# Performance work log

Hardware: AMD Instinct MI355X
Metric: run time of the kernel (lower is better)

Reference implementation:

```python
import jax, jax.numpy as jnp
import numpy as np

B, S, DIM, H = 2, 2048, 1024, 16
HD = DIM // H  # head dim = 64


def setup_inputs() -> dict:
    key = jax.random.key(0)
    ks = jax.random.split(key, 10)
    scale = 1.0 / np.sqrt(DIM)
    x = jax.random.normal(ks[0], (B, S, DIM), dtype=jnp.float32)
    # per-head projection weights stacked over heads: [H, DIM, HD]
    Wq = jax.random.normal(ks[1], (H, DIM, HD), dtype=jnp.float32) * scale
    bq = jax.random.normal(ks[2], (H, HD), dtype=jnp.float32) * 0.01
    Wk = jax.random.normal(ks[3], (H, DIM, HD), dtype=jnp.float32) * scale
    bk = jax.random.normal(ks[4], (H, HD), dtype=jnp.float32) * 0.01
    Wv = jax.random.normal(ks[5], (H, DIM, HD), dtype=jnp.float32) * scale
    bv = jax.random.normal(ks[6], (H, HD), dtype=jnp.float32) * 0.01
    # output linear: [DIM, DIM]
    Wo = jax.random.normal(ks[7], (DIM, DIM), dtype=jnp.float32) * scale
    bo = jax.random.normal(ks[8], (DIM,), dtype=jnp.float32) * 0.01
    return {"x": x, "Wq": Wq, "bq": bq, "Wk": Wk, "bk": bk,
            "Wv": Wv, "bv": bv, "Wo": Wo, "bo": bo}


def reference(x, Wq, bq, Wk, bk, Wv, bv, Wo, bo):
    # per-head projections: [B, H, S, HD]
    q = jnp.einsum('bsd,hde->bhse', x, Wq) + bq[None, :, None, :]
    k = jnp.einsum('bsd,hde->bhse', x, Wk) + bk[None, :, None, :]
    v = jnp.einsum('bsd,hde->bhse', x, Wv) + bv[None, :, None, :]
    # causal attention scores: [B, H, S, S], scaled by sqrt(head_dim)
    scores = jnp.einsum('bhse,bhte->bhst', q, k) / jnp.sqrt(jnp.float32(HD))
    causal = jnp.tril(jnp.ones((S, S), dtype=bool))
    scores = jnp.where(causal[None, None], scores, -jnp.inf)
    attn = jax.nn.softmax(scores, axis=-1)
    out = jnp.einsum('bhst,bhte->bhse', attn, v)  # [B, H, S, HD]
    # concat heads in order -> [B, S, DIM]
    out = out.transpose(0, 2, 1, 3).reshape(B, S, DIM)
    return out @ Wo + bo
```

## Files before the change

### kernel.cpp

```cpp
#include <hip/hip_runtime.h>

typedef _Float16 half8 __attribute__((ext_vector_type(8)));
typedef _Float16 half4 __attribute__((ext_vector_type(4)));
typedef float f32x4 __attribute__((ext_vector_type(4)));

#define MFMA32(a, b, c) __builtin_amdgcn_mfma_f32_16x16x32_f16((a), (b), (c), 0, 0, 0)
#define MFMA16(a, b, c) __builtin_amdgcn_mfma_f32_16x16x16f16((a), (b), (c), 0, 0, 0)

static constexpr int Bc = 2, Sc = 2048, DIMc = 1024, Hc = 16, HDc = 64;
static constexpr int Mc = Bc * Sc;
static constexpr int NQKV = 3 * DIMc;

__device__ __forceinline__ void gl_lds16(const _Float16* g, _Float16* l) {
  __builtin_amdgcn_global_load_lds(
      (const __attribute__((address_space(1))) void*)g,
      (__attribute__((address_space(3))) void*)l, 16, 0, 0);
}


__global__ __launch_bounds__(256) void k_prep_all(
    const float* __restrict__ x, const float* __restrict__ Wq,
    const float* __restrict__ Wk, const float* __restrict__ Wv,
    const float* __restrict__ Wo, _Float16* __restrict__ xh,
    _Float16* __restrict__ WallT, _Float16* __restrict__ WoT) {
  __shared__ float Ls[64 * 65];
  const int bx = blockIdx.x, tid = threadIdx.x;
  if (bx < 16384) {
    int i = bx * 256 + tid;
    xh[i] = (_Float16)x[i];
    return;
  }
  int b2 = bx - 16384;
  if (b2 < 768) {
    const int dt = b2 & 15, ph = b2 >> 4;
    const int p = ph >> 4, h = ph & 15;
    const float* W = (p == 0) ? Wq : (p == 1) ? Wk : Wv;
    for (int c = tid; c < 4096; c += 256) {
      int dr = c >> 6, e = c & 63;
      Ls[e * 65 + dr] = W[h * 65536 + (dt * 64 + dr) * 64 + e];
    }
    __syncthreads();
    for (int c = tid; c < 4096; c += 256) {
      int e = c >> 6, dr = c & 63;
      WallT[(size_t)(p * 1024 + h * 64 + e) * 1024 + dt * 64 + dr] = (_Float16)Ls[e * 65 + dr];
    }
  } else {
    int b3 = b2 - 768;
    const int dt = b3 & 15, nt = b3 >> 4;
    for (int c = tid; c < 4096; c += 256) {
      int dr = c >> 6, nl = c & 63;
      Ls[nl * 65 + dr] = Wo[(dt * 64 + dr) * 1024 + nt * 64 + nl];
    }
    __syncthreads();
    for (int c = tid; c < 4096; c += 256) {
      int nl = c >> 6, dr = c & 63;
      WoT[(size_t)(nt * 64 + nl) * 1024 + dt * 64 + dr] = (_Float16)Ls[nl * 65 + dr];
    }
  }
}


#define GEMM_CORE()                                                            \
  __shared__ _Float16 As[128 * 64];                                            \
  __shared__ _Float16 Bs[128 * 64];                                            \
  const int tid = threadIdx.x;                                                 \
  const int lane = tid & 63, wave = tid >> 6;                                  \
  const int quad = lane >> 4, mr = lane & 15, m7 = mr & 7;                     \
  const int wm = wave >> 1, wn = wave & 1;                                     \
  f32x4 acc[4][4];                                                             \
  for (int i = 0; i < 4; i++)                                                  \
    for (int j = 0; j < 4; j++) acc[i][j] = f32x4{0.f, 0.f, 0.f, 0.f};         \
  for (int k0 = 0; k0 < DIMc; k0 += 64) {                                      \
    __syncthreads();                                                           \
    for (int it = 0; it < 4; ++it) {                                           \
      int idx = it * 256 + tid;                                                \
      int row = idx >> 3, scb = (idx & 7) ^ (row & 7);                         \
      gl_lds16(&A[(size_t)(m0 + row) * DIMc + k0 + scb * 8],                   \
               &As[(it * 256 + wave * 64) * 8]);                               \
    }                                                                          \
    for (int it = 0; it < 4; ++it) {                                           \
      int idx = it * 256 + tid;                                                \
      int row = idx >> 3, scb = (idx & 7) ^ (row & 7);                         \
      gl_lds16(&Bt[(size_t)(n0 + row) * DIMc + k0 + scb * 8],                  \
               &Bs[(it * 256 + wave * 64) * 8]);                               \
    }                                                                          \
    __syncthreads();                                                           \
    for (int kk = 0; kk < 2; ++kk) {                                           \
      half8 af[4], bf[4];                                                      \
      for (int i = 0; i < 4; i++)                                              \
        af[i] = *(const half8*)&As[(wm * 64 + i * 16 + mr) * 64 +              \
                                   (((kk * 4 + quad) ^ m7) * 8)];              \
      for (int i = 0; i < 4; i++)                                              \
        bf[i] = *(const half8*)&Bs[(wn * 64 + i * 16 + mr) * 64 +              \
                                   (((kk * 4 + quad) ^ m7) * 8)];              \
      for (int i = 0; i < 4; i++)                                              \
        for (int j = 0; j < 4; j++) acc[i][j] = MFMA32(af[i], bf[j], acc[i][j]); \
    }                                                                          \
  }

__global__ __launch_bounds__(256) void k_gemm_qkv(
    const _Float16* __restrict__ xh, const _Float16* __restrict__ WallT,
    const float* __restrict__ bq, const float* __restrict__ bk,
    const float* __restrict__ bv, _Float16* __restrict__ qh,
    _Float16* __restrict__ kh, _Float16* __restrict__ vT) {
  const int id = blockIdx.x;
  const bool qkrole = id < 512;
  const _Float16* A;
  const _Float16* Bt;
  int m0, n0;
  if (qkrole) {
    A = xh; Bt = WallT;
    n0 = (id & 15) * 128; m0 = (id >> 4) * 128;
  } else {
    int j = id - 512;
    A = WallT + (size_t)2048 * DIMc; Bt = xh;
    n0 = (j & 31) * 128; m0 = (j >> 5) * 128;
  }
  GEMM_CORE()
  if (qkrole) {
    for (int i = 0; i < 4; i++) {
      for (int j = 0; j < 4; j++) {
        int col = n0 + wn * 64 + j * 16 + mr;
        int p = col >> 10, rem = col & 1023;
        const float* bias = p ? bk : bq;
        _Float16* dst = p ? kh : qh;
        float bb = bias[rem];
        int h = rem >> 6, e = rem & 63;
        for (int r = 0; r < 4; r++) {
          int row = m0 + wm * 64 + i * 16 + quad * 4 + r;
          int b = row >> 11, s = row & 2047;
          dst[(((size_t)(b * Hc + h)) * Sc + s) * HDc + e] = (_Float16)(acc[i][j][r] + bb);
        }
      }
    }
  } else {
    for (int i = 0; i < 4; i++) {
      int rowb = m0 + wm * 64 + i * 16 + quad * 4;
      for (int j = 0; j < 4; j++) {
        int col = n0 + wn * 64 + j * 16 + mr;
        int b = col >> 11, s = col & 2047;
        for (int r = 0; r < 4; r++) {
          int row = rowb + r;
          vT[(size_t)(b * 1024 + row) * Sc + s] = (_Float16)(acc[i][j][r] + bv[row]);
        }
      }
    }
  }
}

__global__ __launch_bounds__(256) void k_gemm_out(
    const _Float16* __restrict__ A, const _Float16* __restrict__ Bt,
    const float* __restrict__ bo, float* __restrict__ out) {
  const int m0 = blockIdx.y * 128, n0 = blockIdx.x * 128;
  GEMM_CORE()
  for (int i = 0; i < 4; i++) {
    for (int j = 0; j < 4; j++) {
      int col = n0 + wn * 64 + j * 16 + mr;
      float bb = bo[col];
      for (int r = 0; r < 4; r++) {
        int row = m0 + wm * 64 + i * 16 + quad * 4 + r;
        out[(size_t)row * DIMc + col] = acc[i][j][r] + bb;
      }
    }
  }
}


__global__ __launch_bounds__(256, 1) void k_attn(
    const _Float16* __restrict__ qg, const _Float16* __restrict__ kg,
    const _Float16* __restrict__ vTg, _Float16* __restrict__ att) {
  const int bid = blockIdx.x;
  const int qt = 31 - (bid >> 5);
  const int bh = bid & 31;
  const int b = bh >> 4, h = bh & 15;
  const int tid = threadIdx.x, w = tid >> 6, lane = tid & 63;
  const int quad = lane >> 4, mr = lane & 15, m7 = mr & 7;
  const size_t base = (size_t)bh * (Sc * HDc);
  const size_t vbase = ((size_t)b * 1024 + h * 64) * Sc;

  __shared__ _Float16 KV[4][2][2][64 * 64];
  __shared__ float Lsh[4][64];

  const int q0 = qt * 64;
  const int myn = (qt >= w) ? ((qt - w) >> 2) + 1 : 0;

  const _Float16 qsc = (_Float16)(0.125f * 1.44269504f);
  half8 aq[4][2];
  for (int qf = 0; qf < 4; ++qf)
    for (int c = 0; c < 2; ++c) {
      half8 v = *(const half8*)&qg[base + (size_t)(q0 + qf * 16 + mr) * 64 + c * 32 + quad * 8];
      for (int j = 0; j < 8; ++j) v[j] = v[j] * qsc;
      aq[qf][c] = v;
    }

  f32x4 o[4][4];
  f32x4 ol[4];
  for (int nf = 0; nf < 4; ++nf)
    for (int qf = 0; qf < 4; ++qf) o[nf][qf] = f32x4{0.f, 0.f, 0.f, 0.f};
  for (int qf = 0; qf < 4; ++qf) ol[qf] = f32x4{0.f, 0.f, 0.f, 0.f};
  const half4 ones = {(_Float16)1.f, (_Float16)1.f, (_Float16)1.f, (_Float16)1.f};

  if (myn > 0) {
    const _Float16* ks = kg + base + (size_t)w * 4096;
    const _Float16* vs = vTg + vbase + w * 64;
    for (int it = 0; it < 8; ++it) {
      int idx = it * 64 + lane;
      int row = idx >> 3, scb = (idx & 7) ^ (row & 7);
      gl_lds16(ks + (size_t)row * 64 + scb * 8, &KV[w][0][0][it * 512]);
    }
    for (int it = 0; it < 8; ++it) {
      int idx = it * 64 + lane;
      int row = idx >> 3, scb = (idx & 7) ^ (row & 7);
      gl_lds16(vs + (size_t)row * Sc + scb * 8, &KV[w][0][1][it * 512]);
    }
  }
  asm volatile("s_waitcnt vmcnt(0)" ::: "memory");

  for (int i = 0; i < myn; ++i) {
    const int t = w + (i << 2);
    const _Float16* Kc = &KV[w][i & 1][0][0];
    const _Float16* Vc = &KV[w][i & 1][1][0];

    if (i + 1 < myn) {
      const _Float16* ks = kg + base + (size_t)(t + 4) * 4096;
      const _Float16* vs = vTg + vbase + (t + 4) * 64;
      _Float16* Kn = &KV[w][(i + 1) & 1][0][0];
      _Float16* Vn = &KV[w][(i + 1) & 1][1][0];
      for (int it = 0; it < 8; ++it) {
        int idx = it * 64 + lane;
        int row = idx >> 3, scb = (idx & 7) ^ (row & 7);
        gl_lds16(ks + (size_t)row * 64 + scb * 8, Kn + it * 512);
      }
      for (int it = 0; it < 8; ++it) {
        int idx = it * 64 + lane;
        int row = idx >> 3, scb = (idx & 7) ^ (row & 7);
        gl_lds16(vs + (size_t)row * Sc + scb * 8, Vn + it * 512);
      }
    }

    const bool diag = (t == qt);
    half4 pf[4][4];
    for (int kf = 0; kf < 4; ++kf) {
      const int r0 = (kf * 16 + mr) * 64;
      half8 k0 = *(const half8*)&Kc[r0 + ((quad ^ m7) * 8)];
      half8 k1 = *(const half8*)&Kc[r0 + (((quad ^ 4) ^ m7) * 8)];
      for (int qf = 0; qf < 4; ++qf) {
        f32x4 z = {0.f, 0.f, 0.f, 0.f};
        z = MFMA32(k0, aq[qf][0], z);
        z = MFMA32(k1, aq[qf][1], z);
        half4 pp;
        const int kvb = kf * 16 + quad * 4;
        for (int r = 0; r < 4; ++r) {
          float p = __builtin_amdgcn_exp2f(z[r]);
          if (diag && (kvb + r > qf * 16 + mr)) p = 0.f;
          pp[r] = (_Float16)p;
        }
        pf[qf][kf] = pp;
      }
    }

    for (int nf = 0; nf < 4; ++nf) {
      const int er = (nf * 16 + mr) * 64;
      for (int kc = 0; kc < 4; ++kc) {
        int kb = kc * 2 + (quad >> 1);
        half4 vv = *(const half4*)&Vc[er + ((kb ^ m7) * 8) + (quad & 1) * 4];
        for (int qf = 0; qf < 4; ++qf) o[nf][qf] = MFMA16(vv, pf[qf][kc], o[nf][qf]);
      }
    }
    for (int kc = 0; kc < 4; ++kc)
      for (int qf = 0; qf < 4; ++qf) ol[qf] = MFMA16(ones, pf[qf][kc], ol[qf]);

    asm volatile("s_waitcnt vmcnt(0)" ::: "memory");
  }

  __syncthreads();
  float* Osh = (float*)&KV[0][0][0][0];
  for (int nf = 0; nf < 4; ++nf)
    for (int qf = 0; qf < 4; ++qf)
      for (int r = 0; r < 4; ++r)
        Osh[w * 4096 + (nf * 16 + quad * 4 + r) * 64 + qf * 16 + mr] = o[nf][qf][r];
  if (quad == 0)
    for (int qf = 0; qf < 4; ++qf) Lsh[w][qf * 16 + mr] = ol[qf][0];
  __syncthreads();

  const int q = tid & 63, e0 = (tid >> 6) * 16;
  const float linv = 1.0f / (Lsh[0][q] + Lsh[1][q] + Lsh[2][q] + Lsh[3][q]);
  half8 o0, o1;
  for (int e = 0; e < 8; ++e) {
    float s = Osh[(e0 + e) * 64 + q] + Osh[4096 + (e0 + e) * 64 + q] +
              Osh[8192 + (e0 + e) * 64 + q] + Osh[12288 + (e0 + e) * 64 + q];
    o0[e] = (_Float16)(s * linv);
  }
  for (int e = 8; e < 16; ++e) {
    float s = Osh[(e0 + e) * 64 + q] + Osh[4096 + (e0 + e) * 64 + q] +
              Osh[8192 + (e0 + e) * 64 + q] + Osh[12288 + (e0 + e) * 64 + q];
    o1[e - 8] = (_Float16)(s * linv);
  }
  const size_t orow = ((size_t)(b * Sc + q0 + q)) * DIMc + h * 64 + e0;
  *(half8*)&att[orow] = o0;
  *(half8*)&att[orow + 8] = o1;
}


extern "C" void kernel_launch(void* const* d_in, const int* in_sizes, int n_in,
                              void* d_out, int out_size, void* d_ws, size_t ws_size,
                              hipStream_t stream) {
  const float* x  = (const float*)d_in[0];
  const float* Wq = (const float*)d_in[1];
  const float* bq = (const float*)d_in[2];
  const float* Wk = (const float*)d_in[3];
  const float* bk = (const float*)d_in[4];
  const float* Wv = (const float*)d_in[5];
  const float* bv = (const float*)d_in[6];
  const float* Wo = (const float*)d_in[7];
  const float* bo = (const float*)d_in[8];
  float* out = (float*)d_out;

  _Float16* p = (_Float16*)d_ws;
  _Float16* xh    = p; p += (size_t)Mc * DIMc;
  _Float16* WallT = p; p += (size_t)NQKV * DIMc;
  _Float16* WoT   = p; p += (size_t)DIMc * DIMc;
  _Float16* qh    = p; p += (size_t)Bc * Hc * Sc * HDc;
  _Float16* kh    = p; p += (size_t)Bc * Hc * Sc * HDc;
  _Float16* vT    = p; p += (size_t)Bc * Hc * Sc * HDc;
  _Float16* atth  = p;

  k_prep_all<<<16384 + 768 + 256, 256, 0, stream>>>(x, Wq, Wk, Wv, Wo, xh, WallT, WoT);
  k_gemm_qkv<<<768, 256, 0, stream>>>(xh, WallT, bq, bk, bv, qh, kh, vT);
  k_attn<<<1024, 256, 0, stream>>>(qh, kh, vT, atth);
  k_gemm_out<<<dim3(DIMc / 128, Mc / 128), 256, 0, stream>>>(atth, WoT, bo, out);
}
```

Measured before the change: 212.3 us.

## Load K/V fragments directly into registers instead of staging through LDS

Attention now reads K and V fragments straight from global memory into registers, with K double-buffered in registers across ping-pong unrolled tiles, instead of async-copying swizzled tiles into LDS. The score/exp and PV MFMAs are interleaved per 16-key chunk, which shrinks the live probability array. LDS use drops to the final reduction buffer and launch bounds allow two blocks per CU, aiming to cut LDS traffic and raise occupancy. In exchange, V loads become strided half4 global reads, and register pressure under the tighter launch bound may cause spills.

```diff
diff --git a/kernel.cpp b/kernel.cpp
--- a/kernel.cpp
+++ b/kernel.cpp
@@ -166,7 +166,44 @@
 }
 
 
-__global__ __launch_bounds__(256, 1) void k_attn(
+#define ATT_TILE(KC, KN, tt)                                                   \
+  {                                                                            \
+    const int t_ = (tt);                                                       \
+    if (t_ + 4 <= qt) {                                                        \
+      for (int kf = 0; kf < 4; ++kf) {                                         \
+        const size_t r_ = (size_t)((t_ + 4) * 64 + kf * 16 + mr) * 64;         \
+        KN[kf][0] = *(const half8*)&Kg[r_ + quad * 8];                         \
+        KN[kf][1] = *(const half8*)&Kg[r_ + 32 + quad * 8];                    \
+      }                                                                        \
+    }                                                                          \
+    half4 vv[4][4];                                                            \
+    for (int nf = 0; nf < 4; ++nf)                                             \
+      for (int kc = 0; kc < 4; ++kc)                                           \
+        vv[nf][kc] = *(const half4*)&Vg[(size_t)(nf * 16 + mr) * Sc +          \
+                                        t_ * 64 + kc * 16 + quad * 4];         \
+    const bool diag = (t_ == qt);                                              \
+    for (int kc = 0; kc < 4; ++kc) {                                           \
+      half4 pf4[4];                                                            \
+      for (int qf = 0; qf < 4; ++qf) {                                         \
+        f32x4 z = {0.f, 0.f, 0.f, 0.f};                                        \
+        z = MFMA32(KC[kc][0], aq[qf][0], z);                                   \
+        z = MFMA32(KC[kc][1], aq[qf][1], z);                                   \
+        half4 pp;                                                              \
+        for (int r = 0; r < 4; ++r) {                                          \
+          float p = __builtin_amdgcn_exp2f(z[r]);                              \
+          if (diag && (kc * 16 + quad * 4 + r > qf * 16 + mr)) p = 0.f;        \
+          pp[r] = (_Float16)p;                                                 \
+        }                                                                      \
+        pf4[qf] = pp;                                                          \
+      }                                                                        \
+      for (int nf = 0; nf < 4; ++nf)                                           \
+        for (int qf = 0; qf < 4; ++qf)                                         \
+          o[nf][qf] = MFMA16(vv[nf][kc], pf4[qf], o[nf][qf]);                  \
+      for (int qf = 0; qf < 4; ++qf) ol[qf] = MFMA16(ones, pf4[qf], ol[qf]);   \
+    }                                                                          \
+  }
+
+__global__ __launch_bounds__(256, 2) void k_attn(
     const _Float16* __restrict__ qg, const _Float16* __restrict__ kg,
     const _Float16* __restrict__ vTg, _Float16* __restrict__ att) {
   const int bid = blockIdx.x;
@@ -174,11 +211,12 @@
   const int bh = bid & 31;
   const int b = bh >> 4, h = bh & 15;
   const int tid = threadIdx.x, w = tid >> 6, lane = tid & 63;
-  const int quad = lane >> 4, mr = lane & 15, m7 = mr & 7;
+  const int quad = lane >> 4, mr = lane & 15;
   const size_t base = (size_t)bh * (Sc * HDc);
-  const size_t vbase = ((size_t)b * 1024 + h * 64) * Sc;
-
-  __shared__ _Float16 KV[4][2][2][64 * 64];
+  const _Float16* Kg = kg + base;
+  const _Float16* Vg = vTg + ((size_t)b * 1024 + h * 64) * Sc;
+
+  __shared__ float Osh[4 * 4096];
   __shared__ float Lsh[4][64];
 
   const int q0 = qt * 64;
@@ -200,81 +238,24 @@
   for (int qf = 0; qf < 4; ++qf) ol[qf] = f32x4{0.f, 0.f, 0.f, 0.f};
   const half4 ones = {(_Float16)1.f, (_Float16)1.f, (_Float16)1.f, (_Float16)1.f};
 
+  half8 kA[4][2], kB[4][2];
   if (myn > 0) {
-    const _Float16* ks = kg + base + (size_t)w * 4096;
-    const _Float16* vs = vTg + vbase + w * 64;
-    for (int it = 0; it < 8; ++it) {
-      int idx = it * 64 + lane;
-      int row = idx >> 3, scb = (idx & 7) ^ (row & 7);
-      gl_lds16(ks + (size_t)row * 64 + scb * 8, &KV[w][0][0][it * 512]);
-    }
-    for (int it = 0; it < 8; ++it) {
-      int idx = it * 64 + lane;
-      int row = idx >> 3, scb = (idx & 7) ^ (row & 7);
-      gl_lds16(vs + (size_t)row * Sc + scb * 8, &KV[w][0][1][it * 512]);
-    }
-  }
-  asm volatile("s_waitcnt vmcnt(0)" ::: "memory");
-
-  for (int i = 0; i < myn; ++i) {
-    const int t = w + (i << 2);
-    const _Float16* Kc = &KV[w][i & 1][0][0];
-    const _Float16* Vc = &KV[w][i & 1][1][0];
-
-    if (i + 1 < myn) {
-      const _Float16* ks = kg + base + (size_t)(t + 4) * 4096;
-      const _Float16* vs = vTg + vbase + (t + 4) * 64;
-      _Float16* Kn = &KV[w][(i + 1) & 1][0][0];
-      _Float16* Vn = &KV[w][(i + 1) & 1][1][0];
-      for (int it = 0; it < 8; ++it) {
-        int idx = it * 64 + lane;
-        int row = idx >> 3, scb = (idx & 7) ^ (row & 7);
-        gl_lds16(ks + (size_t)row * 64 + scb * 8, Kn + it * 512);
-      }
-      for (int it = 0; it < 8; ++it) {
-        int idx = it * 64 + lane;
-        int row = idx >> 3, scb = (idx & 7) ^ (row & 7);
-        gl_lds16(vs + (size_t)row * Sc + scb * 8, Vn + it * 512);
-      }
-    }
-
-    const bool diag = (t == qt);
-    half4 pf[4][4];
     for (int kf = 0; kf < 4; ++kf) {
-      const int r0 = (kf * 16 + mr) * 64;
-      half8 k0 = *(const half8*)&Kc[r0 + ((quad ^ m7) * 8)];
-      half8 k1 = *(const half8*)&Kc[r0 + (((quad ^ 4) ^ m7) * 8)];
-      for (int qf = 0; qf < 4; ++qf) {
-        f32x4 z = {0.f, 0.f, 0.f, 0.f};
-        z = MFMA32(k0, aq[qf][0], z);
-        z = MFMA32(k1, aq[qf][1], z);
-        half4 pp;
-        const int kvb = kf * 16 + quad * 4;
-        for (int r = 0; r < 4; ++r) {
-          float p = __builtin_amdgcn_exp2f(z[r]);
-          if (diag && (kvb + r > qf * 16 + mr)) p = 0.f;
-          pp[r] = (_Float16)p;
-        }
-        pf[qf][kf] = pp;
-      }
-    }
-
-    for (int nf = 0; nf < 4; ++nf) {
-      const int er = (nf * 16 + mr) * 64;
-      for (int kc = 0; kc < 4; ++kc) {
-        int kb = kc * 2 + (quad >> 1);
-        half4 vv = *(const half4*)&Vc[er + ((kb ^ m7) * 8) + (quad & 1) * 4];
-        for (int qf = 0; qf < 4; ++qf) o[nf][qf] = MFMA16(vv, pf[qf][kc], o[nf][qf]);
-      }
-    }
-    for (int kc = 0; kc < 4; ++kc)
-      for (int qf = 0; qf < 4; ++qf) ol[qf] = MFMA16(ones, pf[qf][kc], ol[qf]);
-
-    asm volatile("s_waitcnt vmcnt(0)" ::: "memory");
-  }
-
-  __syncthreads();
-  float* Osh = (float*)&KV[0][0][0][0];
+      const size_t r_ = (size_t)(w * 64 + kf * 16 + mr) * 64;
+      kA[kf][0] = *(const half8*)&Kg[r_ + quad * 8];
+      kA[kf][1] = *(const half8*)&Kg[r_ + 32 + quad * 8];
+    }
+  }
+
+  int i = 0, t = w;
+  for (; i + 2 <= myn; i += 2, t += 8) {
+    ATT_TILE(kA, kB, t)
+    ATT_TILE(kB, kA, t + 4)
+  }
+  if (i < myn) {
+    ATT_TILE(kA, kB, t)
+  }
+
   for (int nf = 0; nf < 4; ++nf)
     for (int qf = 0; qf < 4; ++qf)
       for (int r = 0; r < 4; ++r)
```

Measured after the change: 225.7 us. +6.3%, slower.

## Halve attention KV tile to 32 keys and allow two blocks per CU

Applied to the files above, without the earlier changes.

The attention kernel now stages 32-key K/V tiles per wave instead of 64, which halves the shared-memory footprint. The launch bound rises to two blocks per CU, so more waves are resident to hide latency. The finer key tiles also spread causal work more evenly across the four waves. The causal mask is now computed from the key offset on every tile, and the sync before the output reduction is dropped because each wave's output slot aliases only its own KV region. In exchange there are twice as many loop iterations with smaller MFMA batches and more per-element mask checks.

```diff
diff --git a/kernel.cpp b/kernel.cpp
--- a/kernel.cpp
+++ b/kernel.cpp
@@ -166,7 +166,7 @@
 }
 
 
-__global__ __launch_bounds__(256, 1) void k_attn(
+__global__ __launch_bounds__(256, 2) void k_attn(
     const _Float16* __restrict__ qg, const _Float16* __restrict__ kg,
     const _Float16* __restrict__ vTg, _Float16* __restrict__ att) {
   const int bid = blockIdx.x;
@@ -174,15 +174,17 @@
   const int bh = bid & 31;
   const int b = bh >> 4, h = bh & 15;
   const int tid = threadIdx.x, w = tid >> 6, lane = tid & 63;
-  const int quad = lane >> 4, mr = lane & 15, m7 = mr & 7;
+  const int quad = lane >> 4, mr = lane & 15, m7 = mr & 7, m3 = mr & 3;
   const size_t base = (size_t)bh * (Sc * HDc);
-  const size_t vbase = ((size_t)b * 1024 + h * 64) * Sc;
-
-  __shared__ _Float16 KV[4][2][2][64 * 64];
+  const _Float16* Kg = kg + base;
+  const _Float16* Vg = vTg + ((size_t)b * 1024 + h * 64) * Sc;
+
+  __shared__ _Float16 KV[4][2][2][2048];
   __shared__ float Lsh[4][64];
 
   const int q0 = qt * 64;
-  const int myn = (qt >= w) ? ((qt - w) >> 2) + 1 : 0;
+  const int ntt = 2 * qt + 2;
+  const int myn = (w < ntt) ? ((ntt - 1 - w) >> 2) + 1 : 0;
 
   const _Float16 qsc = (_Float16)(0.125f * 1.44269504f);
   half8 aq[4][2];
@@ -200,47 +202,34 @@
   for (int qf = 0; qf < 4; ++qf) ol[qf] = f32x4{0.f, 0.f, 0.f, 0.f};
   const half4 ones = {(_Float16)1.f, (_Float16)1.f, (_Float16)1.f, (_Float16)1.f};
 
-  if (myn > 0) {
-    const _Float16* ks = kg + base + (size_t)w * 4096;
-    const _Float16* vs = vTg + vbase + w * 64;
-    for (int it = 0; it < 8; ++it) {
-      int idx = it * 64 + lane;
-      int row = idx >> 3, scb = (idx & 7) ^ (row & 7);
-      gl_lds16(ks + (size_t)row * 64 + scb * 8, &KV[w][0][0][it * 512]);
-    }
-    for (int it = 0; it < 8; ++it) {
-      int idx = it * 64 + lane;
-      int row = idx >> 3, scb = (idx & 7) ^ (row & 7);
-      gl_lds16(vs + (size_t)row * Sc + scb * 8, &KV[w][0][1][it * 512]);
-    }
-  }
+#define STAGE32(dst, tt)                                                       \
+  {                                                                            \
+    const _Float16* ks = Kg + (size_t)(tt) * 2048;                             \
+    const _Float16* vs = Vg + (tt) * 32;                                       \
+    for (int it = 0; it < 4; ++it) {                                           \
+      int idx = it * 64 + lane;                                                \
+      int row = idx >> 3, scb = (idx & 7) ^ (row & 7);                         \
+      gl_lds16(ks + (size_t)row * 64 + scb * 8, (dst) + it * 512);             \
+    }                                                                          \
+    for (int it = 0; it < 4; ++it) {                                           \
+      int idx = it * 64 + lane;                                                \
+      int row = idx >> 2, scb = (idx & 3) ^ (row & 3);                         \
+      gl_lds16(vs + (size_t)row * Sc + scb * 8, (dst) + 2048 + it * 512);      \
+    }                                                                          \
+  }
+
+  if (myn > 0) STAGE32(&KV[w][0][0][0], w)
   asm volatile("s_waitcnt vmcnt(0)" ::: "memory");
 
   for (int i = 0; i < myn; ++i) {
-    const int t = w + (i << 2);
+    const int t = w + 4 * i;
     const _Float16* Kc = &KV[w][i & 1][0][0];
     const _Float16* Vc = &KV[w][i & 1][1][0];
-
-    if (i + 1 < myn) {
-      const _Float16* ks = kg + base + (size_t)(t + 4) * 4096;
-      const _Float16* vs = vTg + vbase + (t + 4) * 64;
-      _Float16* Kn = &KV[w][(i + 1) & 1][0][0];
-      _Float16* Vn = &KV[w][(i + 1) & 1][1][0];
-      for (int it = 0; it < 8; ++it) {
-        int idx = it * 64 + lane;
-        int row = idx >> 3, scb = (idx & 7) ^ (row & 7);
-        gl_lds16(ks + (size_t)row * 64 + scb * 8, Kn + it * 512);
-      }
-      for (int it = 0; it < 8; ++it) {
-        int idx = it * 64 + lane;
-        int row = idx >> 3, scb = (idx & 7) ^ (row & 7);
-        gl_lds16(vs + (size_t)row * Sc + scb * 8, Vn + it * 512);
-      }
-    }
-
-    const bool diag = (t == qt);
-    half4 pf[4][4];
-    for (int kf = 0; kf < 4; ++kf) {
+    if (i + 1 < myn) STAGE32(&KV[w][(i + 1) & 1][0][0], t + 4)
+
+    const int dg = (t - 2 * qt) * 32;
+    half4 pf[4][2];
+    for (int kf = 0; kf < 2; ++kf) {
       const int r0 = (kf * 16 + mr) * 64;
       half8 k0 = *(const half8*)&Kc[r0 + ((quad ^ m7) * 8)];
       half8 k1 = *(const half8*)&Kc[r0 + (((quad ^ 4) ^ m7) * 8)];
@@ -249,10 +238,10 @@
         z = MFMA32(k0, aq[qf][0], z);
         z = MFMA32(k1, aq[qf][1], z);
         half4 pp;
-        const int kvb = kf * 16 + quad * 4;
+        const int kvr = dg + kf * 16 + quad * 4;
         for (int r = 0; r < 4; ++r) {
           float p = __builtin_amdgcn_exp2f(z[r]);
-          if (diag && (kvb + r > qf * 16 + mr)) p = 0.f;
+          if (kvr + r > qf * 16 + mr) p = 0.f;
           pp[r] = (_Float16)p;
         }
         pf[qf][kf] = pp;
@@ -260,20 +249,20 @@
     }
 
     for (int nf = 0; nf < 4; ++nf) {
-      const int er = (nf * 16 + mr) * 64;
-      for (int kc = 0; kc < 4; ++kc) {
-        int kb = kc * 2 + (quad >> 1);
-        half4 vv = *(const half4*)&Vc[er + ((kb ^ m7) * 8) + (quad & 1) * 4];
-        for (int qf = 0; qf < 4; ++qf) o[nf][qf] = MFMA16(vv, pf[qf][kc], o[nf][qf]);
-      }
-    }
-    for (int kc = 0; kc < 4; ++kc)
+      const int rb = (nf * 16 + mr) * 32;
+      for (int kc = 0; kc < 2; ++kc) {
+        int ch = kc * 2 + (quad >> 1);
+        half4 vv = *(const half4*)&Vc[rb + ((ch ^ m3) * 8) + (quad & 1) * 4];
+        for (int qf = 0; qf < 4; ++qf)
+          o[nf][qf] = MFMA16(vv, pf[qf][kc], o[nf][qf]);
+      }
+    }
+    for (int kc = 0; kc < 2; ++kc)
       for (int qf = 0; qf < 4; ++qf) ol[qf] = MFMA16(ones, pf[qf][kc], ol[qf]);
 
     asm volatile("s_waitcnt vmcnt(0)" ::: "memory");
   }
 
-  __syncthreads();
   float* Osh = (float*)&KV[0][0][0][0];
   for (int nf = 0; nf < 4; ++nf)
     for (int qf = 0; qf < 4; ++qf)
@@ -299,6 +288,7 @@
   const size_t orow = ((size_t)(b * Sc + q0 + q)) * DIMc + h * 64 + e0;
   *(half8*)&att[orow] = o0;
   *(half8*)&att[orow + 8] = o1;
+#undef STAGE32
 }
 
 
```

After: 195.2 us. 1.09x faster.
